# Kernel optimization log

Hardware: AMD Instinct MI355X
Metric: run time of the kernel (lower is better)

Reference implementation:

```python
import jax, jax.numpy as jnp
import numpy as np

jax.config.update('jax_enable_x64', True)

RES = 0.1
HASH_SIZE = 2 ** 20
D = 120
HEADS = 8
HEAD_DIM = D // HEADS  # 15
MOD_T = 201
BMIN = np.array([-2.6, -8.1, 0.0], dtype=np.float32)
BMAX = np.array([4.6, 4.7, 3.1], dtype=np.float32)
PRIMES = np.array([73856093, 19349669, 83492791], dtype=np.int64)
M = 200000


def _build_buffer():
    axes = [np.arange(BMIN[i], BMAX[i], RES, dtype=np.float32) for i in range(3)]
    g = np.meshgrid(*axes, indexing='ij')
    coords = np.stack(g, axis=-1).reshape(-1, 3)
    n = coords.shape[0]
    grid = np.floor(coords / RES).astype(np.int64)
    h = np.remainder((grid * PRIMES).sum(-1), HASH_SIZE)
    buf = np.full(HASH_SIZE, n, dtype=np.int64)
    # loop assigns in increasing i and keeps the first => min index per hash slot
    np.minimum.at(buf, h, np.arange(n, dtype=np.int64))
    buf = np.where(buf == n, -1, buf)
    return buf, n


def setup_inputs() -> dict:
    key = jax.random.key(0)
    ks = jax.random.split(key, 9)
    buf, n_vox = _build_buffer()
    pts = jnp.asarray(BMIN) + jax.random.uniform(ks[0], (M, 3), dtype=jnp.float32) * jnp.asarray(BMAX - BMIN)
    times = jax.random.randint(ks[1], (M,), 0, 1000, dtype=jnp.int64)
    scale = float(1.0 / np.sqrt(D))
    return {
        'query_pts': pts,
        'query_times': times,
        'buffer_voxel_index': jnp.asarray(buf),
        'static_features': 0.01 * jax.random.normal(ks[2], (n_vox, D), dtype=jnp.float32),
        'dynamic_features': 0.01 * jax.random.normal(ks[3], (n_vox, D), dtype=jnp.float32),
        'time_embeddings': 0.01 * jax.random.normal(ks[4], (MOD_T, D), dtype=jnp.float32),
        'fusion_td_w': scale * jax.random.normal(ks[5], (4, D, D), dtype=jnp.float32),
        'fusion_td_b': jnp.zeros((4, D), dtype=jnp.float32),
        'fusion_sd_w': scale * jax.random.normal(ks[6], (4, D, D), dtype=jnp.float32),
        'fusion_sd_b': jnp.zeros((4, D), dtype=jnp.float32),
    }


def _fusion(a, b, W, B):
    # LocalSelfAttentionFusion: 2-token multi-head self-attention over [a; b],
    # returning the attended first token. W/B stack (q, k, v, out) projections.
    m = a.shape[0]
    tok = jnp.stack([a, b], axis=1)  # [M, 2, D]
    q = (tok @ W[0] + B[0]).reshape(m, 2, HEADS, HEAD_DIM)
    k = (tok @ W[1] + B[1]).reshape(m, 2, HEADS, HEAD_DIM)
    v = (tok @ W[2] + B[2]).reshape(m, 2, HEADS, HEAD_DIM)
    s = jnp.einsum('mqhd,mkhd->mhqk', q, k) * np.float32(1.0 / np.sqrt(HEAD_DIM))
    p = jax.nn.softmax(s, axis=-1)  # [M, H, 2, 2]
    o = jnp.einsum('mhqk,mkhd->mqhd', p, v).reshape(m, 2, D)
    return (o @ W[3] + B[3])[:, 0]  # fused token, [M, D]


def reference(query_pts, query_times, buffer_voxel_index, static_features, dynamic_features,
              time_embeddings, fusion_td_w, fusion_td_b, fusion_sd_w, fusion_sd_b):
    grid = jnp.floor(query_pts / RES).astype(jnp.int64)
    h = jnp.remainder((grid * jnp.asarray(PRIMES)).sum(-1), HASH_SIZE)
    v_idx = buffer_voxel_index[h]              # [M]
    valid = v_idx >= 0
    vi = jnp.where(valid, v_idx, 0)            # safe gather index
    ti = jnp.remainder(query_times, MOD_T)
    sf = static_features[vi]                   # [M, D]
    df = dynamic_features[vi]                  # [M, D]
    te = time_embeddings[ti]                   # [M, D]
    cond = _fusion(df, te, fusion_td_w, fusion_td_b)
    fused = _fusion(sf, cond, fusion_sd_w, fusion_sd_b)
    return jnp.where(valid[:, None], fused, jnp.float32(0))
```

## Files before the change

kernel.cpp:

```cpp
#include <hip/hip_runtime.h>
#include <math.h>

#define DD   120
#define KPAD 128
#define KP   136
#define MT   64
#define NTHR 512
#define HASH_MASK 1048575LL
#define MODT 201

typedef short  short8  __attribute__((ext_vector_type(8)));
typedef float  floatx4 __attribute__((ext_vector_type(4)));

__device__ __forceinline__ unsigned short f2b(float f) {
    __bf16 h = (__bf16)f;
    return __builtin_bit_cast(unsigned short, h);
}
__device__ __forceinline__ float b2f(unsigned short u) {
    unsigned int x = ((unsigned int)u) << 16;
    return __builtin_bit_cast(float, x);
}
template<int CTRL>
__device__ __forceinline__ float dpp_add(float v) {
    int y = __builtin_amdgcn_update_dpp(0, __builtin_bit_cast(int, v),
                                        CTRL, 0xF, 0xF, false);
    return v + __builtin_bit_cast(float, y);
}
__device__ __forceinline__ float rsum16(float v) {
    v = dpp_add<0x128>(v);
    v = dpp_add<0x124>(v);
    v = dpp_add<0x122>(v);
    v = dpp_add<0x121>(v);
    return v;
}
__device__ __forceinline__ uint2 pack4(float4 v) {
    unsigned int lo = (unsigned int)f2b(v.x) | ((unsigned int)f2b(v.y) << 16);
    unsigned int hi = (unsigned int)f2b(v.z) | ((unsigned int)f2b(v.w) << 16);
    return make_uint2(lo, hi);
}

__global__ __launch_bounds__(256)
void prep_weights(const float* __restrict__ td_w, const float* __restrict__ sd_w,
                  unsigned short* __restrict__ wt)
{
    int idx = blockIdx.x * 256 + threadIdx.x;
    int mat = idx >> 14;
    int k   = (idx >> 7) & 127;
    int n   = idx & 127;
    const float* src = (mat < 4) ? (td_w + mat * DD * DD) : (sd_w + (mat - 4) * DD * DD);
    float v = (n < DD && k < DD) ? src[k * DD + n] : 0.f;
    wt[(mat << 14) + (n << 7) + k] = f2b(v);
}

__global__ __launch_bounds__(128)
void prep_te(const float* __restrict__ temb, const float* __restrict__ td_w,
             const float* __restrict__ td_b,
             unsigned short* __restrict__ k1t, unsigned short* __restrict__ v1t)
{
    int t = blockIdx.x;
    int n = threadIdx.x;
    float a1 = 0.f, a2 = 0.f;
    if (n < DD) {
        a1 = td_b[DD + n];
        a2 = td_b[2 * DD + n];
        const float* te = temb + t * DD;
        const float* w1 = td_w + 1 * DD * DD;
        const float* w2 = td_w + 2 * DD * DD;
        for (int k = 0; k < DD; k++) {
            float x = te[k];
            a1 = fmaf(x, w1[k * DD + n], a1);
            a2 = fmaf(x, w2[k * DD + n], a2);
        }
    }
    k1t[t * KPAD + n] = f2b(a1);
    v1t[t * KPAD + n] = f2b(a2);
}

__device__ __forceinline__ void gemm_tile(const unsigned short* IN,
                                          const unsigned short* __restrict__ WT,
                                          const float* __restrict__ bias,
                                          unsigned short* OUT,
                                          int lm, int lq, int n0)
{
    const int n = n0 + lm;
    short8 bfr[4];
#pragma unroll
    for (int ks = 0; ks < 4; ks++)
        bfr[ks] = *(const short8*)(WT + n * KPAD + ks * 32 + lq * 8);
    float bv = (n < DD) ? bias[n] : 0.f;
#pragma unroll
    for (int mt = 0; mt < 4; mt++) {
        floatx4 acc = {0.f, 0.f, 0.f, 0.f};
#pragma unroll
        for (int ks = 0; ks < 4; ks++) {
            short8 a = *(const short8*)(IN + (mt * 16 + lm) * KP + ks * 32 + lq * 8);
            acc = __builtin_amdgcn_mfma_f32_16x16x32_bf16(a, bfr[ks], acc, 0, 0, 0);
        }
#pragma unroll
        for (int r = 0; r < 4; r++)
            OUT[(mt * 16 + lq * 4 + r) * KP + n] = f2b(acc[r] + bv);
    }
}

__device__ __forceinline__ void gemm_out(const unsigned short* IN,
                                         const unsigned short* __restrict__ WT,
                                         const float* __restrict__ bias,
                                         float* __restrict__ out,
                                         const int* s_vr, int pbase, int Mpts,
                                         int lm, int lq, int n0)
{
    const int n = n0 + lm;
    short8 bfr[4];
#pragma unroll
    for (int ks = 0; ks < 4; ks++)
        bfr[ks] = *(const short8*)(WT + n * KPAD + ks * 32 + lq * 8);
    float bv = (n < DD) ? bias[n] : 0.f;
#pragma unroll
    for (int mt = 0; mt < 4; mt++) {
        floatx4 acc = {0.f, 0.f, 0.f, 0.f};
#pragma unroll
        for (int ks = 0; ks < 4; ks++) {
            short8 a = *(const short8*)(IN + (mt * 16 + lm) * KP + ks * 32 + lq * 8);
            acc = __builtin_amdgcn_mfma_f32_16x16x32_bf16(a, bfr[ks], acc, 0, 0, 0);
        }
        if (n < DD) {
#pragma unroll
            for (int r = 0; r < 4; r++) {
                int row = mt * 16 + lq * 4 + r;
                int gp = pbase + row;
                if (gp < Mpts)
                    out[(size_t)gp * DD + n] = (s_vr[row] >= 0) ? (acc[r] + bv) : 0.f;
            }
        }
    }
}

__global__ __launch_bounds__(NTHR, 4)
void voxel_mfma_kernel(const float* __restrict__ pts,
                       const int* __restrict__ times,
                       const int* __restrict__ vox_buf,
                       const float* __restrict__ stat_f,
                       const float* __restrict__ dyn_f,
                       const float* __restrict__ td_b,
                       const float* __restrict__ sd_b,
                       const unsigned short* __restrict__ wt,
                       const unsigned short* __restrict__ k1t,
                       const unsigned short* __restrict__ v1t,
                       float* __restrict__ out,
                       int Mpts)
{
    __shared__ __align__(16) unsigned short sA[MT * KP];
    __shared__ __align__(16) unsigned short sC[MT * KP];
    __shared__ __align__(16) unsigned short sO[MT * KP];
    __shared__ __align__(16) int s_vr[MT];
    __shared__ __align__(16) int s_ti[MT];

    const int tid  = threadIdx.x;
    const int lane = tid & 63;
    const int lm   = lane & 15;
    const int lq   = lane >> 4;
    const int wv   = tid >> 6;
    const int n0h  = wv * 15;
    const int n0t  = wv * 16;
    const int nn   = n0h + lm;
    const int pbase = blockIdx.x * MT;
    const float kscale = 0.37250226f;
    const float msk = (lm < 15) ? 1.f : 0.f;

    {
        const int p   = tid >> 3;
        const int sub = tid & 7;
        const int gp  = pbase + p;
        int vr = -1, ti = 0;
        if (gp < Mpts) {
            float x = pts[3 * gp + 0];
            float y = pts[3 * gp + 1];
            float z = pts[3 * gp + 2];
            long long gx = (long long)floorf(x / 0.1f);
            long long gy = (long long)floorf(y / 0.1f);
            long long gz = (long long)floorf(z / 0.1f);
            long long hh = (gx * 73856093LL + gy * 19349669LL + gz * 83492791LL) & HASH_MASK;
            vr = vox_buf[(int)hh];
            ti = times[gp] % MODT;
        }
        if (sub == 0) { s_vr[p] = vr; s_ti[p] = ti; }
        const int vi = (vr >= 0) ? vr : 0;
        const float* drow = dyn_f + (size_t)vi * DD;
#pragma unroll
        for (int j = 0; j < 4; j++) {
            int f = sub + 8 * j;
            if (f < 30) {
                float4 v = *(const float4*)(drow + f * 4);
                *(uint2*)(sA + p * KP + f * 4) = pack4(v);
            }
        }
        if (sub == 7) {
            *(uint4*)(sA + p * KP + 120) = make_uint4(0u, 0u, 0u, 0u);
            *(uint4*)(sO + p * KP + 120) = make_uint4(0u, 0u, 0u, 0u);
        }
    }
    __syncthreads();

    {
        const unsigned short* w0 = wt + 0 * 16384;
        const unsigned short* w1 = wt + 1 * 16384;
        const unsigned short* w2 = wt + 2 * 16384;
        short8 bq[4], bk[4], bvv[4];
#pragma unroll
        for (int ks = 0; ks < 4; ks++) {
            bq[ks]  = *(const short8*)(w0 + nn * KPAD + ks * 32 + lq * 8);
            bk[ks]  = *(const short8*)(w1 + nn * KPAD + ks * 32 + lq * 8);
            bvv[ks] = *(const short8*)(w2 + nn * KPAD + ks * 32 + lq * 8);
        }
        const float f1bq = td_b[nn];
        const float f1bk = td_b[120 + nn];
        const float f1bv = td_b[240 + nn];
#pragma unroll
        for (int mt = 0; mt < 4; mt++) {
            short8 a[4];
#pragma unroll
            for (int ks = 0; ks < 4; ks++)
                a[ks] = *(const short8*)(sA + (mt * 16 + lm) * KP + ks * 32 + lq * 8);
            int4 tiv = *(const int4*)(&s_ti[mt * 16 + lq * 4]);
            int tt[4] = {tiv.x, tiv.y, tiv.z, tiv.w};
            float k1v[4], v1v[4];
#pragma unroll
            for (int r = 0; r < 4; r++) {
                k1v[r] = b2f(k1t[tt[r] * KPAD + nn]);
                v1v[r] = b2f(v1t[tt[r] * KPAD + nn]);
            }
            floatx4 q = {0.f,0.f,0.f,0.f}, k0 = {0.f,0.f,0.f,0.f}, v0 = {0.f,0.f,0.f,0.f};
#pragma unroll
            for (int ks = 0; ks < 4; ks++) {
                q  = __builtin_amdgcn_mfma_f32_16x16x32_bf16(a[ks], bq[ks],  q,  0, 0, 0);
                k0 = __builtin_amdgcn_mfma_f32_16x16x32_bf16(a[ks], bk[ks],  k0, 0, 0, 0);
                v0 = __builtin_amdgcn_mfma_f32_16x16x32_bf16(a[ks], bvv[ks], v0, 0, 0, 0);
            }
#pragma unroll
            for (int r = 0; r < 4; r++) {
                float qf = (q[r] + f1bq) * msk;
                float c0 = rsum16(qf * (k0[r] + f1bk));
                float c1 = rsum16(qf * k1v[r]);
                float e  = exp2f((c1 - c0) * kscale);
                float p0 = __builtin_amdgcn_rcpf(1.f + e);
                float o  = p0 * (v0[r] + f1bv) + (e * p0) * v1v[r];
                if (lm < 15)
                    sO[(mt * 16 + lq * 4 + r) * KP + nn] = f2b(o);
            }
        }
    }
    __syncthreads();

    {
        float4 g0, g1, g2, g3 = {0.f,0.f,0.f,0.f};
        int a0, a1, a2, a3 = -1;
        {
            int i = tid, p = i / 30, f = i % 30;
            int vi0 = s_vr[p] >= 0 ? s_vr[p] : 0;
            g0 = *(const float4*)(stat_f + (size_t)vi0 * DD + f * 4);
            a0 = p * KP + f * 4;
            i += NTHR; p = i / 30; f = i % 30;
            int vi1 = s_vr[p] >= 0 ? s_vr[p] : 0;
            g1 = *(const float4*)(stat_f + (size_t)vi1 * DD + f * 4);
            a1 = p * KP + f * 4;
            i += NTHR; p = i / 30; f = i % 30;
            int vi2 = s_vr[p] >= 0 ? s_vr[p] : 0;
            g2 = *(const float4*)(stat_f + (size_t)vi2 * DD + f * 4);
            a2 = p * KP + f * 4;
            i += NTHR;
            if (i < MT * 30) {
                p = i / 30; f = i % 30;
                int vi3 = s_vr[p] >= 0 ? s_vr[p] : 0;
                g3 = *(const float4*)(stat_f + (size_t)vi3 * DD + f * 4);
                a3 = p * KP + f * 4;
            }
        }
        gemm_tile(sO, wt + 3 * 16384, td_b + 360, sC, lm, lq, n0t);
        *(uint2*)(sA + a0) = pack4(g0);
        *(uint2*)(sA + a1) = pack4(g1);
        *(uint2*)(sA + a2) = pack4(g2);
        if (a3 >= 0) *(uint2*)(sA + a3) = pack4(g3);
    }
    __syncthreads();

    {
        const unsigned short* u0 = wt + 4 * 16384;
        const unsigned short* u1 = wt + 5 * 16384;
        const unsigned short* u2 = wt + 6 * 16384;
        short8 c1f[4], c2f[4];
#pragma unroll
        for (int ks = 0; ks < 4; ks++) {
            c1f[ks] = *(const short8*)(u1 + nn * KPAD + ks * 32 + lq * 8);
            c2f[ks] = *(const short8*)(u2 + nn * KPAD + ks * 32 + lq * 8);
        }
        const float f2bq = sd_b[nn];
        const float f2bk = sd_b[120 + nn];
        const float f2bv = sd_b[240 + nn];
#pragma unroll
        for (int mt = 0; mt < 4; mt++) {
            short8 a[4], c[4];
#pragma unroll
            for (int ks = 0; ks < 4; ks++) {
                a[ks] = *(const short8*)(sA + (mt * 16 + lm) * KP + ks * 32 + lq * 8);
                c[ks] = *(const short8*)(sC + (mt * 16 + lm) * KP + ks * 32 + lq * 8);
            }
            floatx4 q = {0.f,0.f,0.f,0.f}, k20 = {0.f,0.f,0.f,0.f}, k21 = {0.f,0.f,0.f,0.f};
#pragma unroll
            for (int ks = 0; ks < 4; ks++) {
                short8 b0 = *(const short8*)(u0 + nn * KPAD + ks * 32 + lq * 8);
                q   = __builtin_amdgcn_mfma_f32_16x16x32_bf16(a[ks], b0,      q,   0, 0, 0);
                k20 = __builtin_amdgcn_mfma_f32_16x16x32_bf16(a[ks], c1f[ks], k20, 0, 0, 0);
                k21 = __builtin_amdgcn_mfma_f32_16x16x32_bf16(c[ks], c1f[ks], k21, 0, 0, 0);
            }
            float p0a[4], p1a[4];
#pragma unroll
            for (int r = 0; r < 4; r++) {
                float qf = (q[r] + f2bq) * msk;
                float c0 = rsum16(qf * (k20[r] + f2bk));
                float c1 = rsum16(qf * (k21[r] + f2bk));
                float e  = exp2f((c1 - c0) * kscale);
                p0a[r] = __builtin_amdgcn_rcpf(1.f + e);
                p1a[r] = e * p0a[r];
            }
            floatx4 v20 = {0.f,0.f,0.f,0.f}, v21 = {0.f,0.f,0.f,0.f};
#pragma unroll
            for (int ks = 0; ks < 4; ks++) {
                v20 = __builtin_amdgcn_mfma_f32_16x16x32_bf16(a[ks], c2f[ks], v20, 0, 0, 0);
                v21 = __builtin_amdgcn_mfma_f32_16x16x32_bf16(c[ks], c2f[ks], v21, 0, 0, 0);
            }
#pragma unroll
            for (int r = 0; r < 4; r++) {
                float o = p0a[r] * (v20[r] + f2bv) + p1a[r] * (v21[r] + f2bv);
                if (lm < 15)
                    sO[(mt * 16 + lq * 4 + r) * KP + nn] = f2b(o);
            }
        }
    }
    __syncthreads();

    gemm_out(sO, wt + 7 * 16384, sd_b + 360, out, s_vr, pbase, Mpts, lm, lq, n0t);
}

extern "C" void kernel_launch(void* const* d_in, const int* in_sizes, int n_in,
                              void* d_out, int out_size, void* d_ws, size_t ws_size,
                              hipStream_t stream) {
    const float* pts   = (const float*)d_in[0];
    const int*   times = (const int*)d_in[1];
    const int*   vox   = (const int*)d_in[2];
    const float* statf = (const float*)d_in[3];
    const float* dynf  = (const float*)d_in[4];
    const float* temb  = (const float*)d_in[5];
    const float* td_w  = (const float*)d_in[6];
    const float* td_b  = (const float*)d_in[7];
    const float* sd_w  = (const float*)d_in[8];
    const float* sd_b  = (const float*)d_in[9];

    unsigned short* wt  = (unsigned short*)d_ws;
    unsigned short* k1t = wt + 8 * 128 * 128;
    unsigned short* v1t = k1t + 201 * 128;

    prep_weights<<<512, 256, 0, stream>>>(td_w, sd_w, wt);
    prep_te<<<201, 128, 0, stream>>>(temb, td_w, td_b, k1t, v1t);

    int Mpts = in_sizes[0] / 3;
    int blocks = (Mpts + MT - 1) / MT;
    voxel_mfma_kernel<<<blocks, NTHR, 0, stream>>>(
        pts, times, vox, statf, dynf, td_b, sd_b, wt, k1t, v1t,
        (float*)d_out, Mpts);
}
```

Baseline: 465.6 us.

## Fold first-stage output projection into second-stage K/V weights and drop sC buffer

```diff
diff --git a/kernel.cpp b/kernel.cpp
--- a/kernel.cpp
+++ b/kernel.cpp
@@ -50,6 +50,34 @@
     const float* src = (mat < 4) ? (td_w + mat * DD * DD) : (sd_w + (mat - 4) * DD * DD);
     float v = (n < DD && k < DD) ? src[k * DD + n] : 0.f;
     wt[(mat << 14) + (n << 7) + k] = f2b(v);
+}
+
+__global__ __launch_bounds__(256)
+void prep_fused(const float* __restrict__ td_w, const float* __restrict__ td_b,
+                const float* __restrict__ sd_w, const float* __restrict__ sd_b,
+                unsigned short* __restrict__ wf, float* __restrict__ fb)
+{
+    int idx = blockIdx.x * 256 + threadIdx.x;
+    int mat = idx >> 14;
+    int k   = (idx >> 7) & 127;
+    int n   = idx & 127;
+    const float* W3 = td_w + 3 * DD * DD;
+    const float* Um = sd_w + (mat + 1) * DD * DD;
+    float acc = 0.f;
+    if (n < DD && k < DD) {
+        for (int j = 0; j < DD; j++)
+            acc = fmaf(W3[k * DD + j], Um[j * DD + n], acc);
+    }
+    wf[(mat << 14) + (n << 7) + k] = f2b(acc);
+    if (k == DD) {
+        float s = 0.f;
+        if (n < DD) {
+            s = sd_b[(mat + 1) * DD + n];
+            for (int j = 0; j < DD; j++)
+                s = fmaf(td_b[3 * DD + j], Um[j * DD + n], s);
+        }
+        fb[(mat << 7) + n] = s;
+    }
 }
 
 __global__ __launch_bounds__(128)
@@ -76,32 +104,6 @@
     v1t[t * KPAD + n] = f2b(a2);
 }
 
-__device__ __forceinline__ void gemm_tile(const unsigned short* IN,
-                                          const unsigned short* __restrict__ WT,
-                                          const float* __restrict__ bias,
-                                          unsigned short* OUT,
-                                          int lm, int lq, int n0)
-{
-    const int n = n0 + lm;
-    short8 bfr[4];
-#pragma unroll
-    for (int ks = 0; ks < 4; ks++)
-        bfr[ks] = *(const short8*)(WT + n * KPAD + ks * 32 + lq * 8);
-    float bv = (n < DD) ? bias[n] : 0.f;
-#pragma unroll
-    for (int mt = 0; mt < 4; mt++) {
-        floatx4 acc = {0.f, 0.f, 0.f, 0.f};
-#pragma unroll
-        for (int ks = 0; ks < 4; ks++) {
-            short8 a = *(const short8*)(IN + (mt * 16 + lm) * KP + ks * 32 + lq * 8);
-            acc = __builtin_amdgcn_mfma_f32_16x16x32_bf16(a, bfr[ks], acc, 0, 0, 0);
-        }
-#pragma unroll
-        for (int r = 0; r < 4; r++)
-            OUT[(mt * 16 + lq * 4 + r) * KP + n] = f2b(acc[r] + bv);
-    }
-}
-
 __device__ __forceinline__ void gemm_out(const unsigned short* IN,
                                          const unsigned short* __restrict__ WT,
                                          const float* __restrict__ bias,
@@ -135,7 +137,7 @@
     }
 }
 
-__global__ __launch_bounds__(NTHR, 4)
+__global__ __launch_bounds__(NTHR, 8)
 void voxel_mfma_kernel(const float* __restrict__ pts,
                        const int* __restrict__ times,
                        const int* __restrict__ vox_buf,
@@ -146,11 +148,11 @@
                        const unsigned short* __restrict__ wt,
                        const unsigned short* __restrict__ k1t,
                        const unsigned short* __restrict__ v1t,
+                       const float* __restrict__ fb,
                        float* __restrict__ out,
                        int Mpts)
 {
     __shared__ __align__(16) unsigned short sA[MT * KP];
-    __shared__ __align__(16) unsigned short sC[MT * KP];
     __shared__ __align__(16) unsigned short sO[MT * KP];
     __shared__ __align__(16) int s_vr[MT];
     __shared__ __align__(16) int s_ti[MT];
@@ -160,9 +162,8 @@
     const int lm   = lane & 15;
     const int lq   = lane >> 4;
     const int wv   = tid >> 6;
-    const int n0h  = wv * 15;
+    const int nn   = wv * 15 + lm;
     const int n0t  = wv * 16;
-    const int nn   = n0h + lm;
     const int pbase = blockIdx.x * MT;
     const float kscale = 0.37250226f;
     const float msk = (lm < 15) ? 1.f : 0.f;
@@ -185,13 +186,14 @@
         }
         if (sub == 0) { s_vr[p] = vr; s_ti[p] = ti; }
         const int vi = (vr >= 0) ? vr : 0;
-        const float* drow = dyn_f + (size_t)vi * DD;
+        const float* drow = dyn_f  + (size_t)vi * DD;
+        const float* srow = stat_f + (size_t)vi * DD;
 #pragma unroll
         for (int j = 0; j < 4; j++) {
             int f = sub + 8 * j;
             if (f < 30) {
-                float4 v = *(const float4*)(drow + f * 4);
-                *(uint2*)(sA + p * KP + f * 4) = pack4(v);
+                *(uint2*)(sA + p * KP + f * 4) = pack4(*(const float4*)(drow + f * 4));
+                *(uint2*)(sO + p * KP + f * 4) = pack4(*(const float4*)(srow + f * 4));
             }
         }
         if (sub == 7) {
@@ -236,6 +238,7 @@
                 k0 = __builtin_amdgcn_mfma_f32_16x16x32_bf16(a[ks], bk[ks],  k0, 0, 0, 0);
                 v0 = __builtin_amdgcn_mfma_f32_16x16x32_bf16(a[ks], bvv[ks], v0, 0, 0, 0);
             }
+            float o4[4];
 #pragma unroll
             for (int r = 0; r < 4; r++) {
                 float qf = (q[r] + f1bq) * msk;
@@ -243,81 +246,52 @@
                 float c1 = rsum16(qf * k1v[r]);
                 float e  = exp2f((c1 - c0) * kscale);
                 float p0 = __builtin_amdgcn_rcpf(1.f + e);
-                float o  = p0 * (v0[r] + f1bv) + (e * p0) * v1v[r];
-                if (lm < 15)
-                    sO[(mt * 16 + lq * 4 + r) * KP + nn] = f2b(o);
-            }
-        }
-    }
-    __syncthreads();
+                o4[r] = p0 * (v0[r] + f1bv) + (e * p0) * v1v[r];
+            }
+            __syncthreads();
+            if (lm < 15) {
+#pragma unroll
+                for (int r = 0; r < 4; r++)
+                    sA[(mt * 16 + lq * 4 + r) * KP + nn] = f2b(o4[r]);
+            }
+        }
+    }
 
     {
-        float4 g0, g1, g2, g3 = {0.f,0.f,0.f,0.f};
-        int a0, a1, a2, a3 = -1;
-        {
-            int i = tid, p = i / 30, f = i % 30;
-            int vi0 = s_vr[p] >= 0 ? s_vr[p] : 0;
-            g0 = *(const float4*)(stat_f + (size_t)vi0 * DD + f * 4);
-            a0 = p * KP + f * 4;
-            i += NTHR; p = i / 30; f = i % 30;
-            int vi1 = s_vr[p] >= 0 ? s_vr[p] : 0;
-            g1 = *(const float4*)(stat_f + (size_t)vi1 * DD + f * 4);
-            a1 = p * KP + f * 4;
-            i += NTHR; p = i / 30; f = i % 30;
-            int vi2 = s_vr[p] >= 0 ? s_vr[p] : 0;
-            g2 = *(const float4*)(stat_f + (size_t)vi2 * DD + f * 4);
-            a2 = p * KP + f * 4;
-            i += NTHR;
-            if (i < MT * 30) {
-                p = i / 30; f = i % 30;
-                int vi3 = s_vr[p] >= 0 ? s_vr[p] : 0;
-                g3 = *(const float4*)(stat_f + (size_t)vi3 * DD + f * 4);
-                a3 = p * KP + f * 4;
-            }
-        }
-        gemm_tile(sO, wt + 3 * 16384, td_b + 360, sC, lm, lq, n0t);
-        *(uint2*)(sA + a0) = pack4(g0);
-        *(uint2*)(sA + a1) = pack4(g1);
-        *(uint2*)(sA + a2) = pack4(g2);
-        if (a3 >= 0) *(uint2*)(sA + a3) = pack4(g3);
-    }
-    __syncthreads();
-
-    {
-        const unsigned short* u0 = wt + 4 * 16384;
-        const unsigned short* u1 = wt + 5 * 16384;
-        const unsigned short* u2 = wt + 6 * 16384;
-        short8 c1f[4], c2f[4];
-#pragma unroll
-        for (int ks = 0; ks < 4; ks++) {
-            c1f[ks] = *(const short8*)(u1 + nn * KPAD + ks * 32 + lq * 8);
-            c2f[ks] = *(const short8*)(u2 + nn * KPAD + ks * 32 + lq * 8);
-        }
+        const unsigned short* u0  = wt + 4 * 16384;
+        const unsigned short* u1  = wt + 5 * 16384;
+        const unsigned short* u2  = wt + 6 * 16384;
+        const unsigned short* w31 = wt + 8 * 16384;
+        const unsigned short* w32 = wt + 9 * 16384;
         const float f2bq = sd_b[nn];
         const float f2bk = sd_b[120 + nn];
         const float f2bv = sd_b[240 + nn];
+        const float fbk1 = fb[nn];
+        const float fbv1 = fb[128 + nn];
 #pragma unroll
         for (int mt = 0; mt < 4; mt++) {
-            short8 a[4], c[4];
+            short8 a[4], s[4];
 #pragma unroll
             for (int ks = 0; ks < 4; ks++) {
                 a[ks] = *(const short8*)(sA + (mt * 16 + lm) * KP + ks * 32 + lq * 8);
-                c[ks] = *(const short8*)(sC + (mt * 16 + lm) * KP + ks * 32 + lq * 8);
+                s[ks] = *(const short8*)(sO + (mt * 16 + lm) * KP + ks * 32 + lq * 8);
             }
             floatx4 q = {0.f,0.f,0.f,0.f}, k20 = {0.f,0.f,0.f,0.f}, k21 = {0.f,0.f,0.f,0.f};
 #pragma unroll
             for (int ks = 0; ks < 4; ks++) {
-                short8 b0 = *(const short8*)(u0 + nn * KPAD + ks * 32 + lq * 8);
-                q   = __builtin_amdgcn_mfma_f32_16x16x32_bf16(a[ks], b0,      q,   0, 0, 0);
-                k20 = __builtin_amdgcn_mfma_f32_16x16x32_bf16(a[ks], c1f[ks], k20, 0, 0, 0);
-                k21 = __builtin_amdgcn_mfma_f32_16x16x32_bf16(c[ks], c1f[ks], k21, 0, 0, 0);
+                short8 b0 = *(const short8*)(u0  + nn * KPAD + ks * 32 + lq * 8);
+                short8 b1 = *(const short8*)(u1  + nn * KPAD + ks * 32 + lq * 8);
+                short8 bw = *(const short8*)(w31 + nn * KPAD + ks * 32 + lq * 8);
+                q   = __builtin_amdgcn_mfma_f32_16x16x32_bf16(s[ks], b0, q,   0, 0, 0);
+                k20 = __builtin_amdgcn_mfma_f32_16x16x32_bf16(s[ks], b1, k20, 0, 0, 0);
+                k21 = __builtin_amdgcn_mfma_f32_16x16x32_bf16(a[ks], bw, k21, 0, 0, 0);
             }
             float p0a[4], p1a[4];
 #pragma unroll
             for (int r = 0; r < 4; r++) {
                 float qf = (q[r] + f2bq) * msk;
                 float c0 = rsum16(qf * (k20[r] + f2bk));
-                float c1 = rsum16(qf * (k21[r] + f2bk));
+                float c1 = rsum16(qf * (k21[r] + fbk1));
                 float e  = exp2f((c1 - c0) * kscale);
                 p0a[r] = __builtin_amdgcn_rcpf(1.f + e);
                 p1a[r] = e * p0a[r];
@@ -325,20 +299,26 @@
             floatx4 v20 = {0.f,0.f,0.f,0.f}, v21 = {0.f,0.f,0.f,0.f};
 #pragma unroll
             for (int ks = 0; ks < 4; ks++) {
-                v20 = __builtin_amdgcn_mfma_f32_16x16x32_bf16(a[ks], c2f[ks], v20, 0, 0, 0);
-                v21 = __builtin_amdgcn_mfma_f32_16x16x32_bf16(c[ks], c2f[ks], v21, 0, 0, 0);
-            }
-#pragma unroll
-            for (int r = 0; r < 4; r++) {
-                float o = p0a[r] * (v20[r] + f2bv) + p1a[r] * (v21[r] + f2bv);
-                if (lm < 15)
-                    sO[(mt * 16 + lq * 4 + r) * KP + nn] = f2b(o);
+                short8 b2  = *(const short8*)(u2  + nn * KPAD + ks * 32 + lq * 8);
+                short8 bw2 = *(const short8*)(w32 + nn * KPAD + ks * 32 + lq * 8);
+                v20 = __builtin_amdgcn_mfma_f32_16x16x32_bf16(s[ks], b2,  v20, 0, 0, 0);
+                v21 = __builtin_amdgcn_mfma_f32_16x16x32_bf16(a[ks], bw2, v21, 0, 0, 0);
+            }
+            float o4[4];
+#pragma unroll
+            for (int r = 0; r < 4; r++)
+                o4[r] = p0a[r] * (v20[r] + f2bv) + p1a[r] * (v21[r] + fbv1);
+            __syncthreads();
+            if (lm < 15) {
+#pragma unroll
+                for (int r = 0; r < 4; r++)
+                    sA[(mt * 16 + lq * 4 + r) * KP + nn] = f2b(o4[r]);
             }
         }
     }
     __syncthreads();
 
-    gemm_out(sO, wt + 7 * 16384, sd_b + 360, out, s_vr, pbase, Mpts, lm, lq, n0t);
+    gemm_out(sA, wt + 7 * 16384, sd_b + 360, out, s_vr, pbase, Mpts, lm, lq, n0t);
 }
 
 extern "C" void kernel_launch(void* const* d_in, const int* in_sizes, int n_in,
@@ -356,15 +336,17 @@
     const float* sd_b  = (const float*)d_in[9];
 
     unsigned short* wt  = (unsigned short*)d_ws;
-    unsigned short* k1t = wt + 8 * 128 * 128;
+    unsigned short* k1t = wt + 10 * 128 * 128;
     unsigned short* v1t = k1t + 201 * 128;
+    float*          fb  = (float*)(v1t + 201 * 128);
 
     prep_weights<<<512, 256, 0, stream>>>(td_w, sd_w, wt);
+    prep_fused<<<128, 256, 0, stream>>>(td_w, td_b, sd_w, sd_b, wt + 8 * 16384, fb);
     prep_te<<<201, 128, 0, stream>>>(temb, td_w, td_b, k1t, v1t);
 
     int Mpts = in_sizes[0] / 3;
     int blocks = (Mpts + MT - 1) / MT;
     voxel_mfma_kernel<<<blocks, NTHR, 0, stream>>>(
-        pts, times, vox, statf, dynf, td_b, sd_b, wt, k1t, v1t,
+        pts, times, vox, statf, dynf, td_b, sd_b, wt, k1t, v1t, fb,
         (float*)d_out, Mpts);
 }
```

Result: slower. 688.4 us (+47.8%).
